# Performance work log

Hardware: AMD Instinct MI355X
Metric: run time of the kernel (lower is better)

Reference implementation:

```python
import jax, jax.numpy as jnp
import numpy as np

B, P, E, D, A = 128, 196, 2048, 512, 512


def setup_inputs() -> dict:
    key = jax.random.key(0)
    ks = jax.random.split(key, 8)
    s = lambda fan_in: 1.0 / np.sqrt(fan_in)
    return {
        "encoder_out": jax.random.normal(ks[0], (B, P, E), jnp.float32),
        "decoder_hidden": jax.random.normal(ks[1], (B, D), jnp.float32),
        "We": jax.random.uniform(ks[2], (E, A), jnp.float32, -s(E), s(E)),
        "be": jax.random.uniform(ks[3], (A,), jnp.float32, -s(E), s(E)),
        "Wd": jax.random.uniform(ks[4], (D, A), jnp.float32, -s(D), s(D)),
        "bd": jax.random.uniform(ks[5], (A,), jnp.float32, -s(D), s(D)),
        "Wf": jax.random.uniform(ks[6], (A, 1), jnp.float32, -s(A), s(A)),
        "bf": jax.random.uniform(ks[7], (1,), jnp.float32, -s(A), s(A)),
    }


def reference(encoder_out, decoder_hidden, We, be, Wd, bd, Wf, bf):
    # att1: [B, P, A]
    att1 = jnp.einsum("bpe,ea->bpa", encoder_out, We) + be
    # att2: [B, A]
    att2 = decoder_hidden @ Wd + bd
    # additive attention scores: [B, P]
    att = (jax.nn.relu(att1 + att2[:, None, :]) @ Wf + bf)[..., 0]
    alpha = jax.nn.softmax(att, axis=1)  # softmax over pixels
    # weighted sum over pixels: [B, E]
    awe = jnp.einsum("bpe,bp->be", encoder_out, alpha)
    return awe, alpha
```

## Files before the change

### kernel.cpp

```cpp
#include <hip/hip_runtime.h>
#include <hip/hip_bf16.h>

typedef __attribute__((ext_vector_type(2))) unsigned int u32x2;
typedef __attribute__((ext_vector_type(4))) float f32x4;
typedef __attribute__((ext_vector_type(4))) unsigned int u32x4;
typedef __attribute__((ext_vector_type(8))) short s16x8;

#define B_  128
#define P_  196
#define E_  2048
#define D_  512
#define A_  512
#define M_  (B_*P_)

typedef __attribute__((address_space(1))) const unsigned int gu32;
typedef __attribute__((address_space(3))) unsigned int lu32;
__device__ __forceinline__ void gl_lds16(const void* g, void* l) {
  __builtin_amdgcn_global_load_lds((gu32*)g, (lu32*)l, 16, 0, 0);
}

#define WAIT_VM3() asm volatile("s_waitcnt vmcnt(3)" ::: "memory")
#define WAIT_VM0() asm volatile("s_waitcnt vmcnt(0)" ::: "memory")
#define WAIT_LGKM0() asm volatile("s_waitcnt lgkmcnt(0)" ::: "memory")

__global__ void we_conv_kernel(const float* __restrict__ We,
                               unsigned short* __restrict__ WeTs) {
  __shared__ float tile[32][33];
  const int tx = threadIdx.x, ty = threadIdx.y;
  const int a0 = blockIdx.x * 32, e0 = blockIdx.y * 32;
  tile[ty][tx] = We[(e0 + ty) * A_ + a0 + tx];
  __syncthreads();
  const float v = tile[tx][ty];
  const unsigned int u = __float_as_uint(v);
  const unsigned short r = (unsigned short)((u + 0x7fffu + ((u >> 16) & 1u)) >> 16);
  const int a = a0 + ty;
  const int kt = blockIdx.y;
  const int c8 = tx >> 3, j = tx & 7;
  const int dest = ((a * 32 + c8 * 8) ^ ((a & 7) << 3)) + j;
  WeTs[kt * 16384 + dest] = r;
}

__global__ void att2_kernel(const float* __restrict__ h, const float* __restrict__ Wd,
                            const float* __restrict__ bd, const float* __restrict__ be,
                            float* __restrict__ att2pb) {
  const int b = blockIdx.x;
  const int t = threadIdx.x;
  __shared__ float hs[D_];
  hs[t] = h[b * D_ + t];
  hs[t + 256] = h[b * D_ + t + 256];
  __syncthreads();
  float a0 = 0.f, a1 = 0.f;
  for (int d = 0; d < D_; ++d) {
    const float hv = hs[d];
    a0 = fmaf(hv, Wd[d * A_ + t], a0);
    a1 = fmaf(hv, Wd[d * A_ + t + 256], a1);
  }
  att2pb[b * A_ + t] = a0 + bd[t] + be[t];
  att2pb[b * A_ + t + 256] = a1 + bd[t + 256] + be[t + 256];
}

__device__ inline unsigned pk2(float a, float b) {
  union { __hip_bfloat162 h; unsigned u; } cv;
  cv.h = __float22bfloat162_rn(make_float2(a, b));
  return cv.u;
}

__launch_bounds__(1024, 4)
__global__ void score_kernel(const float* __restrict__ enc,
                             const unsigned short* __restrict__ WeTs,
                             const float* __restrict__ att2pb,
                             const float* __restrict__ Wf,
                             float* __restrict__ att_part) {
  __shared__ unsigned short Bh[3][512 * 32];
  __shared__ unsigned short Ahs[3][128 * 32];

  const int bid = blockIdx.x;
  const int m0 = bid * 128;

  const int t = threadIdx.x;
  const int lane = t & 63, w = t >> 6;
  const int wm = (w >> 2) * 32;
  const int wn = (w & 3) * 128;

  const int ar = t >> 3, ac4 = t & 7;
  const float* aptr = enc + (size_t)(m0 + ar) * E_ + ac4 * 4;
  const int awz = (ar * 32 + ac4 * 4) ^ ((ar & 7) << 3);

  const int doff = t * 8;

  const int q = lane >> 4, fr = lane & 15;
  const int fx = (fr & 7) << 3;
  int fa[2], fb[8];
#pragma unroll
  for (int i = 0; i < 2; ++i) fa[i] = ((wm + i * 16 + fr) * 32 + q * 8) ^ fx;
#pragma unroll
  for (int j = 0; j < 8; ++j) fb[j] = ((wn + j * 16 + fr) * 32 + q * 8) ^ fx;

  const f32x4 zero = {0.f, 0.f, 0.f, 0.f};
  f32x4 acc[2][8];
#pragma unroll
  for (int mi = 0; mi < 2; ++mi)
#pragma unroll
    for (int ni = 0; ni < 8; ++ni) acc[mi][ni] = zero;

  unsigned short *bAc = &Ahs[0][0], *bA1 = &Ahs[1][0], *bA2 = &Ahs[2][0];
  unsigned short *bBc = &Bh[0][0],  *bB1 = &Bh[1][0],  *bB2 = &Bh[2][0];

  f32x4 aC, aN;

  {
    aC = *(const f32x4*)(aptr);
    gl_lds16(WeTs + doff, bBc + doff);
    gl_lds16(WeTs + 8192 + doff, bBc + 8192 + doff);
    aN = *(const f32x4*)(aptr + 32);
    gl_lds16(WeTs + 16384 + doff, bB1 + doff);
    gl_lds16(WeTs + 16384 + 8192 + doff, bB1 + 8192 + doff);
    u32x2 av; av[0] = pk2(aC[0], aC[1]); av[1] = pk2(aC[2], aC[3]);
    *(u32x2*)(bAc + awz) = av;
    aC = aN;
    WAIT_VM3();
    WAIT_LGKM0();
    __builtin_amdgcn_s_barrier();
  }

  for (int it = 0; it < 62; ++it) {
    const int kof = (it + 2) * 32;
    aN = *(const f32x4*)(aptr + kof);
    const unsigned short* sb = WeTs + (size_t)(it + 2) * 16384;
    gl_lds16(sb + doff, bB2 + doff);
    gl_lds16(sb + 8192 + doff, bB2 + 8192 + doff);

    {
      u32x2 av; av[0] = pk2(aC[0], aC[1]); av[1] = pk2(aC[2], aC[3]);
      *(u32x2*)(bA1 + awz) = av;
    }
    aC = aN;

    s16x8 fah[2], fbh[4];
    fah[0] = *(const s16x8*)(bAc + fa[0]);
    fah[1] = *(const s16x8*)(bAc + fa[1]);
#pragma unroll
    for (int j = 0; j < 4; ++j) fbh[j] = *(const s16x8*)(bBc + fb[j]);
    __builtin_amdgcn_s_setprio(1);
#pragma unroll
    for (int mi = 0; mi < 2; ++mi)
#pragma unroll
      for (int ni = 0; ni < 4; ++ni)
        acc[mi][ni] = __builtin_amdgcn_mfma_f32_16x16x32_bf16(fah[mi], fbh[ni], acc[mi][ni], 0, 0, 0);
    __builtin_amdgcn_s_setprio(0);
#pragma unroll
    for (int j = 0; j < 4; ++j) fbh[j] = *(const s16x8*)(bBc + fb[4 + j]);
    __builtin_amdgcn_s_setprio(1);
#pragma unroll
    for (int mi = 0; mi < 2; ++mi)
#pragma unroll
      for (int ni = 0; ni < 4; ++ni)
        acc[mi][4 + ni] = __builtin_amdgcn_mfma_f32_16x16x32_bf16(fah[mi], fbh[ni], acc[mi][4 + ni], 0, 0, 0);
    __builtin_amdgcn_s_setprio(0);

    WAIT_VM3();
    WAIT_LGKM0();
    __builtin_amdgcn_s_barrier();

    unsigned short* tmp;
    tmp = bAc; bAc = bA1; bA1 = bA2; bA2 = tmp;
    tmp = bBc; bBc = bB1; bB1 = bB2; bB2 = tmp;
  }

  {
    u32x2 av; av[0] = pk2(aC[0], aC[1]); av[1] = pk2(aC[2], aC[3]);
    *(u32x2*)(bA1 + awz) = av;
    s16x8 fah[2], fbh[4];
    fah[0] = *(const s16x8*)(bAc + fa[0]);
    fah[1] = *(const s16x8*)(bAc + fa[1]);
#pragma unroll
    for (int j = 0; j < 4; ++j) fbh[j] = *(const s16x8*)(bBc + fb[j]);
#pragma unroll
    for (int mi = 0; mi < 2; ++mi)
#pragma unroll
      for (int ni = 0; ni < 4; ++ni)
        acc[mi][ni] = __builtin_amdgcn_mfma_f32_16x16x32_bf16(fah[mi], fbh[ni], acc[mi][ni], 0, 0, 0);
#pragma unroll
    for (int j = 0; j < 4; ++j) fbh[j] = *(const s16x8*)(bBc + fb[4 + j]);
#pragma unroll
    for (int mi = 0; mi < 2; ++mi)
#pragma unroll
      for (int ni = 0; ni < 4; ++ni)
        acc[mi][4 + ni] = __builtin_amdgcn_mfma_f32_16x16x32_bf16(fah[mi], fbh[ni], acc[mi][4 + ni], 0, 0, 0);
    WAIT_VM0();
    WAIT_LGKM0();
    __builtin_amdgcn_s_barrier();
  }

  {
    s16x8 fah[2], fbh[4];
    fah[0] = *(const s16x8*)(bA1 + fa[0]);
    fah[1] = *(const s16x8*)(bA1 + fa[1]);
#pragma unroll
    for (int j = 0; j < 4; ++j) fbh[j] = *(const s16x8*)(bB1 + fb[j]);
#pragma unroll
    for (int mi = 0; mi < 2; ++mi)
#pragma unroll
      for (int ni = 0; ni < 4; ++ni)
        acc[mi][ni] = __builtin_amdgcn_mfma_f32_16x16x32_bf16(fah[mi], fbh[ni], acc[mi][ni], 0, 0, 0);
#pragma unroll
    for (int j = 0; j < 4; ++j) fbh[j] = *(const s16x8*)(bB1 + fb[4 + j]);
#pragma unroll
    for (int mi = 0; mi < 2; ++mi)
#pragma unroll
      for (int ni = 0; ni < 4; ++ni)
        acc[mi][4 + ni] = __builtin_amdgcn_mfma_f32_16x16x32_bf16(fah[mi], fbh[ni], acc[mi][4 + ni], 0, 0, 0);
  }

  const int colL = wn + fr;
  float wfv[8];
#pragma unroll
  for (int ni = 0; ni < 8; ++ni) wfv[ni] = Wf[colL + ni * 16];
#pragma unroll
  for (int mi = 0; mi < 2; ++mi) {
    const int rowb = m0 + wm + mi * 16 + (q << 2);
#pragma unroll
    for (int r = 0; r < 4; ++r) {
      const int row = rowb + r;
      const int bb = row / P_;
      const float* a2 = att2pb + bb * A_ + colL;
      float s = 0.f;
#pragma unroll
      for (int ni = 0; ni < 8; ++ni)
        s += fmaxf(acc[mi][ni][r] + a2[ni * 16], 0.f) * wfv[ni];
#pragma unroll
      for (int off = 1; off < 16; off <<= 1) s += __shfl_xor(s, off);
      if (fr == 0) att_part[row * 4 + (w & 3)] = s;
    }
  }
}

__global__ void softmax_awe_kernel(const float* __restrict__ enc,
                                   const float* __restrict__ att_part,
                                   float* __restrict__ out) {
  const int bid = blockIdx.x;
  const int b = bid >> 1, ch = bid & 1;
  const int t = threadIdx.x;
  __shared__ float sm[256];
  __shared__ float alpha_s[P_];

  float av = -1e30f;
  if (t < P_) {
    const float* apt = att_part + (b * P_ + t) * 4;
    av = (apt[0] + apt[1]) + (apt[2] + apt[3]);
  }
  sm[t] = av;
  __syncthreads();
  for (int st = 128; st > 0; st >>= 1) {
    if (t < st) sm[t] = fmaxf(sm[t], sm[t + st]);
    __syncthreads();
  }
  const float mx = sm[0];
  __syncthreads();
  float ev = 0.f;
  if (t < P_) ev = __expf(av - mx);
  sm[t] = ev;
  __syncthreads();
  for (int st = 128; st > 0; st >>= 1) {
    if (t < st) sm[t] += sm[t + st];
    __syncthreads();
  }
  const float denom = sm[0];
  const float al = ev / denom;
  if (t < P_) {
    alpha_s[t] = al;
    if (ch == 0) out[B_ * E_ + b * P_ + t] = al;
  }
  __syncthreads();

  const int e0 = ch * 1024 + t * 4;
  const float* ebase = enc + (size_t)b * P_ * E_ + e0;
  f32x4 acc = {0.f, 0.f, 0.f, 0.f};
  for (int p = 0; p < P_; ++p) {
    const f32x4 v = *(const f32x4*)(ebase + (size_t)p * E_);
    const float a = alpha_s[p];
    acc.x += a * v.x; acc.y += a * v.y; acc.z += a * v.z; acc.w += a * v.w;
  }
  *(f32x4*)(out + b * E_ + e0) = acc;
}

extern "C" void kernel_launch(void* const* d_in, const int* in_sizes, int n_in,
                              void* d_out, int out_size, void* d_ws, size_t ws_size,
                              hipStream_t stream) {
  const float* enc = (const float*)d_in[0];
  const float* h   = (const float*)d_in[1];
  const float* We  = (const float*)d_in[2];
  const float* be  = (const float*)d_in[3];
  const float* Wd  = (const float*)d_in[4];
  const float* bd  = (const float*)d_in[5];
  const float* Wf  = (const float*)d_in[6];
  float* out = (float*)d_out;

  float* att2pb = (float*)d_ws;
  float* att_part = att2pb + B_ * A_;
  unsigned short* WeTs = (unsigned short*)(att_part + M_ * 4);

  we_conv_kernel<<<dim3(A_ / 32, E_ / 32), dim3(32, 32), 0, stream>>>(We, WeTs);
  att2_kernel<<<B_, 256, 0, stream>>>(h, Wd, bd, be, att2pb);
  score_kernel<<<M_ / 128, 1024, 0, stream>>>(enc, WeTs, att2pb, Wf, att_part);
  softmax_awe_kernel<<<B_ * 2, 256, 0, stream>>>(enc, att_part, out);
}
```

Measured before the change: 142.9 us.

## Retile score GEMM to 112-row blocks with waves splitting only the N dimension

The score GEMM now uses 112-row M tiles (M_=25088 divides evenly by 112, giving 224 blocks instead of 196). Each of the 16 waves covers all 7 M-subtiles and a 32-column N slice, replacing the old 2x8 wave layout. The att_part partial buffer grows to 16 partials per row, which the softmax kernel sums. The MFMA compute now runs before the A-tile LDS store. The intent is to spread the work over more blocks so the CUs stay busy. The cost is more LDS A-fragment reads per MFMA, more partial-sum traffic, and 16 idle A-load rows that are clamped to a valid row.

```diff
diff --git a/kernel.cpp b/kernel.cpp
--- a/kernel.cpp
+++ b/kernel.cpp
@@ -12,6 +12,7 @@
 #define D_  512
 #define A_  512
 #define M_  (B_*P_)
+#define MT  112
 
 typedef __attribute__((address_space(1))) const unsigned int gu32;
 typedef __attribute__((address_space(3))) unsigned int lu32;
@@ -64,6 +65,10 @@
   cv.h = __float22bfloat162_rn(make_float2(a, b));
   return cv.u;
 }
+__device__ __forceinline__ s16x8 ldsr(const unsigned short* p) {
+  return *(const s16x8*)p;
+}
+#define MF(a, b, c) c = __builtin_amdgcn_mfma_f32_16x16x32_bf16(a, b, c, 0, 0, 0)
 
 __launch_bounds__(1024, 4)
 __global__ void score_kernel(const float* __restrict__ enc,
@@ -75,33 +80,34 @@
   __shared__ unsigned short Ahs[3][128 * 32];
 
   const int bid = blockIdx.x;
-  const int m0 = bid * 128;
+  const int m0 = bid * MT;
 
   const int t = threadIdx.x;
   const int lane = t & 63, w = t >> 6;
-  const int wm = (w >> 2) * 32;
-  const int wn = (w & 3) * 128;
+  const int wn = w * 32;
 
   const int ar = t >> 3, ac4 = t & 7;
-  const float* aptr = enc + (size_t)(m0 + ar) * E_ + ac4 * 4;
+  const int arc = ar < MT ? ar : MT - 1;
+  const float* aptr = enc + (size_t)(m0 + arc) * E_ + ac4 * 4;
   const int awz = (ar * 32 + ac4 * 4) ^ ((ar & 7) << 3);
 
   const int doff = t * 8;
 
   const int q = lane >> 4, fr = lane & 15;
   const int fx = (fr & 7) << 3;
-  int fa[2], fb[8];
-#pragma unroll
-  for (int i = 0; i < 2; ++i) fa[i] = ((wm + i * 16 + fr) * 32 + q * 8) ^ fx;
-#pragma unroll
-  for (int j = 0; j < 8; ++j) fb[j] = ((wn + j * 16 + fr) * 32 + q * 8) ^ fx;
+  int fa[7], fb[2];
+#pragma unroll
+  for (int i = 0; i < 7; ++i) fa[i] = ((i * 16 + fr) * 32 + q * 8) ^ fx;
+#pragma unroll
+  for (int j = 0; j < 2; ++j) fb[j] = ((wn + j * 16 + fr) * 32 + q * 8) ^ fx;
 
   const f32x4 zero = {0.f, 0.f, 0.f, 0.f};
-  f32x4 acc[2][8];
-#pragma unroll
-  for (int mi = 0; mi < 2; ++mi)
-#pragma unroll
-    for (int ni = 0; ni < 8; ++ni) acc[mi][ni] = zero;
+  f32x4 acc[7][2];
+#pragma unroll
+  for (int mi = 0; mi < 7; ++mi) {
+    acc[mi][0] = zero;
+    acc[mi][1] = zero;
+  }
 
   unsigned short *bAc = &Ahs[0][0], *bA1 = &Ahs[1][0], *bA2 = &Ahs[2][0];
   unsigned short *bBc = &Bh[0][0],  *bB1 = &Bh[1][0],  *bB2 = &Bh[2][0];
@@ -131,32 +137,23 @@
     gl_lds16(sb + 8192 + doff, bB2 + 8192 + doff);
 
     {
+      s16x8 fbh0 = ldsr(bBc + fb[0]);
+      s16x8 fbh1 = ldsr(bBc + fb[1]);
+      __builtin_amdgcn_s_setprio(1);
+#pragma unroll
+      for (int mi = 0; mi < 7; ++mi) {
+        const s16x8 fah = ldsr(bAc + fa[mi]);
+        MF(fah, fbh0, acc[mi][0]);
+        MF(fah, fbh1, acc[mi][1]);
+      }
+      __builtin_amdgcn_s_setprio(0);
+    }
+
+    {
       u32x2 av; av[0] = pk2(aC[0], aC[1]); av[1] = pk2(aC[2], aC[3]);
       *(u32x2*)(bA1 + awz) = av;
     }
     aC = aN;
-
-    s16x8 fah[2], fbh[4];
-    fah[0] = *(const s16x8*)(bAc + fa[0]);
-    fah[1] = *(const s16x8*)(bAc + fa[1]);
-#pragma unroll
-    for (int j = 0; j < 4; ++j) fbh[j] = *(const s16x8*)(bBc + fb[j]);
-    __builtin_amdgcn_s_setprio(1);
-#pragma unroll
-    for (int mi = 0; mi < 2; ++mi)
-#pragma unroll
-      for (int ni = 0; ni < 4; ++ni)
-        acc[mi][ni] = __builtin_amdgcn_mfma_f32_16x16x32_bf16(fah[mi], fbh[ni], acc[mi][ni], 0, 0, 0);
-    __builtin_amdgcn_s_setprio(0);
-#pragma unroll
-    for (int j = 0; j < 4; ++j) fbh[j] = *(const s16x8*)(bBc + fb[4 + j]);
-    __builtin_amdgcn_s_setprio(1);
-#pragma unroll
-    for (int mi = 0; mi < 2; ++mi)
-#pragma unroll
-      for (int ni = 0; ni < 4; ++ni)
-        acc[mi][4 + ni] = __builtin_amdgcn_mfma_f32_16x16x32_bf16(fah[mi], fbh[ni], acc[mi][4 + ni], 0, 0, 0);
-    __builtin_amdgcn_s_setprio(0);
 
     WAIT_VM3();
     WAIT_LGKM0();
@@ -168,69 +165,47 @@
   }
 
   {
+    s16x8 fbh0 = ldsr(bBc + fb[0]);
+    s16x8 fbh1 = ldsr(bBc + fb[1]);
+#pragma unroll
+    for (int mi = 0; mi < 7; ++mi) {
+      const s16x8 fah = ldsr(bAc + fa[mi]);
+      MF(fah, fbh0, acc[mi][0]);
+      MF(fah, fbh1, acc[mi][1]);
+    }
     u32x2 av; av[0] = pk2(aC[0], aC[1]); av[1] = pk2(aC[2], aC[3]);
     *(u32x2*)(bA1 + awz) = av;
-    s16x8 fah[2], fbh[4];
-    fah[0] = *(const s16x8*)(bAc + fa[0]);
-    fah[1] = *(const s16x8*)(bAc + fa[1]);
-#pragma unroll
-    for (int j = 0; j < 4; ++j) fbh[j] = *(const s16x8*)(bBc + fb[j]);
-#pragma unroll
-    for (int mi = 0; mi < 2; ++mi)
-#pragma unroll
-      for (int ni = 0; ni < 4; ++ni)
-        acc[mi][ni] = __builtin_amdgcn_mfma_f32_16x16x32_bf16(fah[mi], fbh[ni], acc[mi][ni], 0, 0, 0);
-#pragma unroll
-    for (int j = 0; j < 4; ++j) fbh[j] = *(const s16x8*)(bBc + fb[4 + j]);
-#pragma unroll
-    for (int mi = 0; mi < 2; ++mi)
-#pragma unroll
-      for (int ni = 0; ni < 4; ++ni)
-        acc[mi][4 + ni] = __builtin_amdgcn_mfma_f32_16x16x32_bf16(fah[mi], fbh[ni], acc[mi][4 + ni], 0, 0, 0);
     WAIT_VM0();
     WAIT_LGKM0();
     __builtin_amdgcn_s_barrier();
   }
 
   {
-    s16x8 fah[2], fbh[4];
-    fah[0] = *(const s16x8*)(bA1 + fa[0]);
-    fah[1] = *(const s16x8*)(bA1 + fa[1]);
-#pragma unroll
-    for (int j = 0; j < 4; ++j) fbh[j] = *(const s16x8*)(bB1 + fb[j]);
-#pragma unroll
-    for (int mi = 0; mi < 2; ++mi)
-#pragma unroll
-      for (int ni = 0; ni < 4; ++ni)
-        acc[mi][ni] = __builtin_amdgcn_mfma_f32_16x16x32_bf16(fah[mi], fbh[ni], acc[mi][ni], 0, 0, 0);
-#pragma unroll
-    for (int j = 0; j < 4; ++j) fbh[j] = *(const s16x8*)(bB1 + fb[4 + j]);
-#pragma unroll
-    for (int mi = 0; mi < 2; ++mi)
-#pragma unroll
-      for (int ni = 0; ni < 4; ++ni)
-        acc[mi][4 + ni] = __builtin_amdgcn_mfma_f32_16x16x32_bf16(fah[mi], fbh[ni], acc[mi][4 + ni], 0, 0, 0);
+    s16x8 fbh0 = ldsr(bB1 + fb[0]);
+    s16x8 fbh1 = ldsr(bB1 + fb[1]);
+#pragma unroll
+    for (int mi = 0; mi < 7; ++mi) {
+      const s16x8 fah = ldsr(bA1 + fa[mi]);
+      MF(fah, fbh0, acc[mi][0]);
+      MF(fah, fbh1, acc[mi][1]);
+    }
   }
 
   const int colL = wn + fr;
-  float wfv[8];
-#pragma unroll
-  for (int ni = 0; ni < 8; ++ni) wfv[ni] = Wf[colL + ni * 16];
-#pragma unroll
-  for (int mi = 0; mi < 2; ++mi) {
-    const int rowb = m0 + wm + mi * 16 + (q << 2);
+  const float wf0 = Wf[colL], wf1 = Wf[colL + 16];
+#pragma unroll
+  for (int mi = 0; mi < 7; ++mi) {
+    const int rowb = m0 + mi * 16 + (q << 2);
 #pragma unroll
     for (int r = 0; r < 4; ++r) {
       const int row = rowb + r;
       const int bb = row / P_;
       const float* a2 = att2pb + bb * A_ + colL;
-      float s = 0.f;
-#pragma unroll
-      for (int ni = 0; ni < 8; ++ni)
-        s += fmaxf(acc[mi][ni][r] + a2[ni * 16], 0.f) * wfv[ni];
+      float s = fmaxf(acc[mi][0][r] + a2[0], 0.f) * wf0
+              + fmaxf(acc[mi][1][r] + a2[16], 0.f) * wf1;
 #pragma unroll
       for (int off = 1; off < 16; off <<= 1) s += __shfl_xor(s, off);
-      if (fr == 0) att_part[row * 4 + (w & 3)] = s;
+      if (fr == 0) att_part[row * 16 + w] = s;
     }
   }
 }
@@ -246,8 +221,11 @@
 
   float av = -1e30f;
   if (t < P_) {
-    const float* apt = att_part + (b * P_ + t) * 4;
-    av = (apt[0] + apt[1]) + (apt[2] + apt[3]);
+    const float* apt = att_part + (b * P_ + t) * 16;
+    float s = 0.f;
+#pragma unroll
+    for (int i = 0; i < 16; ++i) s += apt[i];
+    av = s;
   }
   sm[t] = av;
   __syncthreads();
@@ -298,10 +276,10 @@
 
   float* att2pb = (float*)d_ws;
   float* att_part = att2pb + B_ * A_;
-  unsigned short* WeTs = (unsigned short*)(att_part + M_ * 4);
+  unsigned short* WeTs = (unsigned short*)(att_part + M_ * 16);
 
   we_conv_kernel<<<dim3(A_ / 32, E_ / 32), dim3(32, 32), 0, stream>>>(We, WeTs);
   att2_kernel<<<B_, 256, 0, stream>>>(h, Wd, bd, be, att2pb);
-  score_kernel<<<M_ / 128, 1024, 0, stream>>>(enc, WeTs, att2pb, Wf, att_part);
+  score_kernel<<<M_ / MT, 1024, 0, stream>>>(enc, WeTs, att2pb, Wf, att_part);
   softmax_awe_kernel<<<B_ * 2, 256, 0, stream>>>(enc, att_part, out);
 }
```

Measured after the change: 130.2 us. -8.9%, faster.
